# Performance work log

Measured on AMD Instinct MI355X. Metric: run time of the kernel, lower is better.

## Reference

```python
import jax, jax.numpy as jnp
import numpy as np

B, C, H, W, K = 16, 313, 128, 128, 5


def setup_inputs() -> dict:
    key = jax.random.key(0)
    k1, k2, k3, k4, k5, k6 = jax.random.split(key, 6)
    pred = jax.random.normal(k1, (B, C, H, W), dtype=jnp.float32)
    _color = jax.random.normal(k2, (B, 2, H, W), dtype=jnp.float32)
    binned_color = jax.random.randint(k3, (B, 1, H, W), 0, C, dtype=jnp.int64)
    knn_idx = jax.random.randint(k4, (C, K), 0, C, dtype=jnp.int64)
    knn_weights = jax.random.uniform(k5, (C, K), dtype=jnp.float32)
    # soft-encoding weights per bin normally sum to 1; normalize for realism
    knn_weights = knn_weights / jnp.sum(knn_weights, axis=1, keepdims=True)
    weights = jax.random.uniform(k6, (C,), dtype=jnp.float32)
    return {
        "pred": pred,
        "_color": _color,
        "binned_color": binned_color,
        "knn_idx": knn_idx,
        "knn_weights": knn_weights,
        "weights": weights,
    }


def reference(pred, _color, binned_color, knn_idx, knn_weights, weights):
    # log_softmax over the C bin channels: (B, C, H, W)
    logp = jax.nn.log_softmax(pred, axis=1)
    target_idx = binned_color[:, 0]                 # (B, H, W)
    idx = knn_idx[target_idx]                       # (B, H, W, K)
    wts = knn_weights[target_idx]                   # (B, H, W, K)
    w = weights[target_idx]                         # (B, H, W)
    idx_bkhw = jnp.transpose(idx, (0, 3, 1, 2))     # (B, K, H, W)
    wts_bkhw = jnp.transpose(wts, (0, 3, 1, 2))     # (B, K, H, W)
    p = jnp.take_along_axis(logp, idx_bkhw, axis=1)  # gather K bins per pixel
    loss = -jnp.mean(jnp.sum(p * wts_bkhw, axis=1) * w)
    return loss
```

## Files before the change

### kernel.cpp

```cpp
#include <hip/hip_runtime.h>


#define CC   313
#define HW   16384
#define NPIX 262144
#define KK   5

__global__ __launch_bounds__(256) void bcl_kernel(
    const float* __restrict__ pred,
    const int*   __restrict__ binned,
    const int*   __restrict__ knn_idx,
    const float* __restrict__ knn_w,
    const float* __restrict__ weights,
    float*       __restrict__ out)
{
    const int tid  = blockIdx.x * blockDim.x + threadIdx.x;
    const int lane = threadIdx.x & 63;
    const int wv   = tid >> 6;
    const int q    = lane >> 5;
    const int sub  = lane & 31;

    const int pb = wv * 128 + sub * 4;
    const int b  = pb >> 14;
    const int hw = pb & (HW - 1);

    const int4 t4 = *(const int4*)(binned + pb);
    const int t[4] = {t4.x, t4.y, t4.z, t4.w};

    int   ki[4][KK];
    float kw[4][KK];
    #pragma unroll
    for (int j = 0; j < 4; ++j) {
        #pragma unroll
        for (int k = 0; k < KK; ++k) {
            ki[j][k] = knn_idx[t[j] * KK + k];
            kw[j][k] = knn_w [t[j] * KK + k];
        }
    }

    const float* base = pred + (size_t)b * CC * HW + hw;

    float s[4]   = {0.f, 0.f, 0.f, 0.f};
    float dot[4] = {0.f, 0.f, 0.f, 0.f};

    for (int c = q; c < CC; c += 2) {
        const float4 x = *(const float4*)(base + (size_t)c * HW);
        const float xv[4] = {x.x, x.y, x.z, x.w};
        #pragma unroll
        for (int j = 0; j < 4; ++j) {
            s[j] += __expf(xv[j]);
            float wsel = (c == ki[j][0]) ? kw[j][0] :
                         (c == ki[j][1]) ? kw[j][1] :
                         (c == ki[j][2]) ? kw[j][2] :
                         (c == ki[j][3]) ? kw[j][3] :
                         (c == ki[j][4]) ? kw[j][4] : 0.0f;
            dot[j] = fmaf(xv[j], wsel, dot[j]);
        }
    }

    float tv = 0.0f;
    #pragma unroll
    for (int j = 0; j < 4; ++j) {
        const float st = s[j]   + __shfl_xor(s[j],   32);
        const float dt = dot[j] + __shfl_xor(dot[j], 32);
        if (q == 0) {
            const float sumw = kw[j][0] + kw[j][1] + kw[j][2] + kw[j][3] + kw[j][4];
            const float val  = dt - logf(st) * sumw;
            tv += val * weights[t[j]];
        }
    }

    #pragma unroll
    for (int off = 32; off > 0; off >>= 1)
        tv += __shfl_down(tv, off);

    __shared__ float red[4];
    if (lane == 0) red[threadIdx.x >> 6] = tv;
    __syncthreads();
    if (threadIdx.x == 0) {
        const float bs = red[0] + red[1] + red[2] + red[3];
        atomicAdd(out, bs * (-1.0f / (float)NPIX));
    }
}

extern "C" void kernel_launch(void* const* d_in, const int* in_sizes, int n_in,
                              void* d_out, int out_size, void* d_ws, size_t ws_size,
                              hipStream_t stream) {
    const float* pred    = (const float*)d_in[0];
    const int*   binned  = (const int*)  d_in[2];
    const int*   knn_idx = (const int*)  d_in[3];
    const float* knn_w   = (const float*)d_in[4];
    const float* weights = (const float*)d_in[5];
    float* out = (float*)d_out;

    hipMemsetAsync(out, 0, sizeof(float), stream);

    bcl_kernel<<<512, 256, 0, stream>>>(pred, binned, knn_idx, knn_w, weights, out);
}
```

Baseline: 454.2 us.

## Split channel loop across 8 lane groups per wave and quadruple grid size

Each wave now covers 32 pixels instead of 128, with 8 lane groups striding the channel dimension by 8 rather than 2. The grid grows from 512 to 2048 blocks, and the loop is manually unrolled two-wide to put more loads in flight. The aim is more parallelism and occupancy for this memory-bound streaming read over roughly 335 MB of predictions. In exchange, each float4 read now covers only 128 contiguous bytes per channel row, and the final cross-lane reduction needs more shuffles.

```diff
diff --git a/kernel.cpp b/kernel.cpp
--- a/kernel.cpp
+++ b/kernel.cpp
@@ -6,7 +6,7 @@
 #define NPIX 262144
 #define KK   5
 
-__global__ __launch_bounds__(256) void bcl_kernel(
+__global__ __launch_bounds__(256, 4) void bcl_kernel(
     const float* __restrict__ pred,
     const int*   __restrict__ binned,
     const int*   __restrict__ knn_idx,
@@ -17,10 +17,10 @@
     const int tid  = blockIdx.x * blockDim.x + threadIdx.x;
     const int lane = threadIdx.x & 63;
     const int wv   = tid >> 6;
-    const int q    = lane >> 5;
-    const int sub  = lane & 31;
+    const int q    = lane >> 3;
+    const int sub  = lane & 7;
 
-    const int pb = wv * 128 + sub * 4;
+    const int pb = wv * 32 + sub * 4;
     const int b  = pb >> 14;
     const int hw = pb & (HW - 1);
 
@@ -43,26 +43,38 @@
     float s[4]   = {0.f, 0.f, 0.f, 0.f};
     float dot[4] = {0.f, 0.f, 0.f, 0.f};
 
-    for (int c = q; c < CC; c += 2) {
-        const float4 x = *(const float4*)(base + (size_t)c * HW);
-        const float xv[4] = {x.x, x.y, x.z, x.w};
-        #pragma unroll
-        for (int j = 0; j < 4; ++j) {
-            s[j] += __expf(xv[j]);
-            float wsel = (c == ki[j][0]) ? kw[j][0] :
-                         (c == ki[j][1]) ? kw[j][1] :
-                         (c == ki[j][2]) ? kw[j][2] :
-                         (c == ki[j][3]) ? kw[j][3] :
-                         (c == ki[j][4]) ? kw[j][4] : 0.0f;
-            dot[j] = fmaf(xv[j], wsel, dot[j]);
-        }
+#define BODY(CIDX)                                                          \
+    {                                                                       \
+        const int cc = (CIDX);                                              \
+        const float4 x = *(const float4*)(base + (size_t)cc * HW);          \
+        const float xv[4] = {x.x, x.y, x.z, x.w};                           \
+        _Pragma("unroll")                                                   \
+        for (int j = 0; j < 4; ++j) {                                       \
+            s[j] += __expf(xv[j]);                                          \
+            float wsel = (cc == ki[j][0]) ? kw[j][0] :                      \
+                         (cc == ki[j][1]) ? kw[j][1] :                      \
+                         (cc == ki[j][2]) ? kw[j][2] :                      \
+                         (cc == ki[j][3]) ? kw[j][3] :                      \
+                         (cc == ki[j][4]) ? kw[j][4] : 0.0f;                \
+            dot[j] = fmaf(xv[j], wsel, dot[j]);                             \
+        }                                                                   \
     }
+
+    int c = q;
+    for (; c + 8 < CC; c += 16) {
+        BODY(c);
+        BODY(c + 8);
+    }
+    if (c < CC) BODY(c);
+#undef BODY
 
     float tv = 0.0f;
     #pragma unroll
     for (int j = 0; j < 4; ++j) {
-        const float st = s[j]   + __shfl_xor(s[j],   32);
-        const float dt = dot[j] + __shfl_xor(dot[j], 32);
+        float st = s[j], dt = dot[j];
+        st += __shfl_xor(st, 8);  dt += __shfl_xor(dt, 8);
+        st += __shfl_xor(st, 16); dt += __shfl_xor(dt, 16);
+        st += __shfl_xor(st, 32); dt += __shfl_xor(dt, 32);
         if (q == 0) {
             const float sumw = kw[j][0] + kw[j][1] + kw[j][2] + kw[j][3] + kw[j][4];
             const float val  = dt - logf(st) * sumw;
@@ -95,5 +107,5 @@
 
     hipMemsetAsync(out, 0, sizeof(float), stream);
 
-    bcl_kernel<<<512, 256, 0, stream>>>(pred, binned, knn_idx, knn_w, weights, out);
+    bcl_kernel<<<2048, 256, 0, stream>>>(pred, binned, knn_idx, knn_w, weights, out);
 }
```

New measurement: 445.5 us. No clear change (-1.9%).
